# Optimization experiments

Hardware: AMD Instinct MI355X
Metric: run time of the kernel (lower is better)

## Reference

```python
import jax, jax.numpy as jnp
import numpy as np

NUM_HEADS = 16
NEG_INF = -1e24


def setup_inputs() -> dict:
    key = jax.random.key(0)
    k1, k2, k3, k4 = jax.random.split(key, 4)
    T, B, E = 2048, 2, 1024
    std = 0.02
    return {
        "x": jax.random.normal(k1, (T, B, E), dtype=jnp.float32),
        "in_proj_weight": jax.random.normal(k2, (3 * E, E), dtype=jnp.float32) * std,
        "in_proj_bias": jnp.zeros((3 * E,), dtype=jnp.float32),
        "out_w": jax.random.normal(k3, (E, E), dtype=jnp.float32) * std,
        "out_b": jnp.zeros((E,), dtype=jnp.float32),
        "key_padding_mask": jax.random.randint(k4, (T, B), 0, 2) > 0,
    }


def reference(x, in_proj_weight, in_proj_bias, out_w, out_b, key_padding_mask):
    # x: [T, B, E]  (Time x Batch x Channel), self-attention (qkv_same path)
    T, B, E = x.shape
    H = NUM_HEADS
    hd = E // H
    scaling = hd ** -0.5
    qkv = jnp.einsum("tbe,fe->tbf", x, in_proj_weight) + in_proj_bias  # [T,B,3E]
    q, k, v = jnp.split(qkv, 3, axis=-1)
    q = (q * scaling).reshape(T, B, H, hd)
    k = k.reshape(T, B, H, hd)
    v = v.reshape(T, B, H, hd)
    # attention scores: [B, H, T(tgt), S(src)]
    scores = jnp.einsum("tbhd,sbhd->bhts", q, k)
    # key_padding_mask: [S, B] -> broadcast over [B, 1, 1, S]
    pad = key_padding_mask.T[:, None, None, :]
    scores = jnp.where(pad, jnp.float32(NEG_INF), scores)
    attn_weights = jax.nn.softmax(scores, axis=-1)
    # dropout p=0.0 in eval -> identity
    attn = jnp.einsum("bhts,sbhd->tbhd", attn_weights, v).reshape(T, B, E)
    out = jnp.einsum("tbe,fe->tbf", attn, out_w) + out_b
    return out
```

## Files before the change

### kernel.cpp

```cpp
#include <hip/hip_runtime.h>
#include <math.h>

#define T_    2048
#define B_    2
#define E_    1024
#define H_    16
#define HD_   64
#define KD_   1024
#define N3_   3072
#define M_    4096
#define NEGI  -1e24f

typedef __attribute__((ext_vector_type(8))) short          bf16x8;
typedef __attribute__((ext_vector_type(4))) float          f32x4;
typedef __attribute__((ext_vector_type(8))) unsigned short u16x8;

__device__ __forceinline__ unsigned short f2bf(float x) {
    unsigned int u = __float_as_uint(x);
    return (unsigned short)((u + 0x7fffu + ((u >> 16) & 1u)) >> 16);
}

__device__ __forceinline__ void gload16(const unsigned short* g, unsigned short* s) {
    __builtin_amdgcn_global_load_lds(
        (const __attribute__((address_space(1))) void*)g,
        (__attribute__((address_space(3))) void*)s, 16, 0, 0);
}

__global__ __launch_bounds__(256) void cvt_bf16(const float* __restrict__ s,
                                                unsigned short* __restrict__ d, int n4) {
    int i = blockIdx.x * 256 + threadIdx.x;
    if (i >= n4) return;
    float4 v = ((const float4*)s)[i];
    ushort4 o;
    o.x = f2bf(v.x); o.y = f2bf(v.y); o.z = f2bf(v.z); o.w = f2bf(v.w);
    ((ushort4*)d)[i] = o;
}

__global__ __launch_bounds__(256) void build_msk(const int* __restrict__ m,
                                                 float* __restrict__ o) {
    int i = blockIdx.x * 256 + threadIdx.x;
    if (i >= T_ * B_) return;
    o[(i & 1) * T_ + (i >> 1)] = m[i] ? NEGI : 0.f;
}

template <int EPI>
__global__ __launch_bounds__(256) void gemm_mfma(
    const unsigned short* __restrict__ A, const unsigned short* __restrict__ W,
    const float* __restrict__ bias,
    unsigned short* __restrict__ q_o, unsigned short* __restrict__ k_o,
    unsigned short* __restrict__ v_o, float* __restrict__ f_o)
{
    __shared__ __align__(16) unsigned short Ab[128 * 64];
    __shared__ __align__(16) unsigned short Bb[128 * 64];
    const int tid = threadIdx.x;
    const int l = tid & 63, w = tid >> 6;
    const int lr = l & 15, g = l >> 4;
    const int m0 = blockIdx.y * 128, n0 = blockIdx.x * 128;
    const int wr = (w >> 1) * 64, wc = (w & 1) * 64;

    f32x4 acc[4][4];
    #pragma unroll
    for (int i = 0; i < 4; ++i)
        #pragma unroll
        for (int j = 0; j < 4; ++j) acc[i][j] = f32x4{0.f, 0.f, 0.f, 0.f};

    for (int k0 = 0; k0 < KD_; k0 += 64) {
        __syncthreads();
        #pragma unroll
        for (int i = 0; i < 4; ++i) {
            const int fb  = (i * 4 + w) * 64;
            const int row = (fb + l) >> 3;
            const int col = ((l & 7) ^ (row & 7)) * 8;
            gload16(&A[(size_t)(m0 + row) * KD_ + k0 + col], &Ab[fb * 8]);
            gload16(&W[(size_t)(n0 + row) * KD_ + k0 + col], &Bb[fb * 8]);
        }
        __syncthreads();
        #pragma unroll
        for (int ks = 0; ks < 2; ++ks) {
            bf16x8 af[4], bf[4];
            #pragma unroll
            for (int mi = 0; mi < 4; ++mi) {
                const int row = wr + mi * 16 + lr;
                af[mi] = *(const bf16x8*)&Ab[row * 64 + (((ks * 4 + g) ^ (row & 7)) * 8)];
            }
            #pragma unroll
            for (int ni = 0; ni < 4; ++ni) {
                const int row = wc + ni * 16 + lr;
                bf[ni] = *(const bf16x8*)&Bb[row * 64 + (((ks * 4 + g) ^ (row & 7)) * 8)];
            }
            #pragma unroll
            for (int mi = 0; mi < 4; ++mi)
                #pragma unroll
                for (int ni = 0; ni < 4; ++ni)
                    acc[mi][ni] = __builtin_amdgcn_mfma_f32_16x16x32_bf16(
                        af[mi], bf[ni], acc[mi][ni], 0, 0, 0);
        }
    }

    if (EPI == 0) {
        const int sec = n0 >> 10;
        unsigned short* dst = (sec == 0) ? q_o : (sec == 1) ? k_o : v_o;
        const float sc = (sec == 0) ? 0.125f : 1.f;
        #pragma unroll
        for (int ni = 0; ni < 4; ++ni) {
            const int fcol = n0 + wc + ni * 16 + lr;
            const int h = (fcol >> 6) & 15, d = fcol & 63;
            const float bv = bias[fcol];
            #pragma unroll
            for (int mi = 0; mi < 4; ++mi)
                #pragma unroll
                for (int p = 0; p < 4; ++p) {
                    const int m = m0 + wr + mi * 16 + g * 4 + p;
                    const int t = m >> 1, b = m & 1;
                    dst[((size_t)(b * H_ + h) * T_ + t) * HD_ + d] =
                        f2bf((acc[mi][ni][p] + bv) * sc);
                }
        }
    } else {
        #pragma unroll
        for (int ni = 0; ni < 4; ++ni) {
            const int fcol = n0 + wc + ni * 16 + lr;
            const float bv = bias[fcol];
            #pragma unroll
            for (int mi = 0; mi < 4; ++mi)
                #pragma unroll
                for (int p = 0; p < 4; ++p) {
                    const int m = m0 + wr + mi * 16 + g * 4 + p;
                    f_o[(size_t)m * E_ + fcol] = acc[mi][ni][p] + bv;
                }
        }
    }
}

__global__ __launch_bounds__(256) void transpose64(const unsigned short* __restrict__ v,
                                                   unsigned short* __restrict__ vt)
{
    __shared__ __align__(16) unsigned short tile[64][72];
    const int bh = blockIdx.y, t0 = blockIdx.x * 64;
    const int tid = threadIdx.x;
    const int r = tid >> 2, c0 = (tid & 3) * 16;
    const unsigned short* src = v + ((size_t)bh * T_ + t0 + r) * HD_ + c0;
    *(u16x8*)&tile[r][c0]     = *(const u16x8*)&src[0];
    *(u16x8*)&tile[r][c0 + 8] = *(const u16x8*)&src[8];
    __syncthreads();
    u16x8 a, b;
    #pragma unroll
    for (int j = 0; j < 8; ++j) a[j] = tile[c0 + j][r];
    #pragma unroll
    for (int j = 0; j < 8; ++j) b[j] = tile[c0 + 8 + j][r];
    unsigned short* dq = vt + ((size_t)bh * HD_ + r) * T_ + t0 + c0;
    *(u16x8*)&dq[0] = a;
    *(u16x8*)&dq[8] = b;
}

__device__ __forceinline__ void stage64(const unsigned short* src, int ld,
                                        unsigned short* buf, int w, int l) {
    #pragma unroll
    for (int c = 0; c < 2; ++c) {
        const int fb  = (c * 4 + w) * 64;
        const int row = (fb + l) >> 3;
        const int col = ((l & 7) ^ (row & 7)) * 8;
        gload16(src + (size_t)row * ld + col, buf + fb * 8);
    }
}

__global__ __launch_bounds__(256, 3) void attn_mfma(
    const unsigned short* __restrict__ qw, const unsigned short* __restrict__ kw,
    const unsigned short* __restrict__ vtw, const float* __restrict__ msk,
    unsigned short* __restrict__ attn)
{
    __shared__ __align__(16) unsigned short Kb[2][64 * 64];
    __shared__ __align__(16) unsigned short Vb[2][64 * 64];
    __shared__ __align__(16) unsigned short Pb[4][32 * 64];

    const int tid = threadIdx.x;
    const int l = tid & 63, w = tid >> 6;
    const int lr = l & 15, g = l >> 4;
    const int bh = blockIdx.y, b = bh >> 4, h = bh & 15;
    const int q0 = blockIdx.x * 128 + w * 32;

    const unsigned short* kb  = kw  + (size_t)bh * T_ * HD_;
    const unsigned short* vtb = vtw + (size_t)bh * HD_ * T_;
    const float* mb = msk + b * T_;
    unsigned short* Pw = Pb[w];

    bf16x8 qf[2][2];
    #pragma unroll
    for (int qc = 0; qc < 2; ++qc) {
        const unsigned short* qrow = qw + ((size_t)bh * T_ + q0 + qc * 16 + lr) * HD_;
        qf[qc][0] = *(const bf16x8*)&qrow[g * 8];
        qf[qc][1] = *(const bf16x8*)&qrow[32 + g * 8];
    }

    f32x4 o[2][4];
    #pragma unroll
    for (int qc = 0; qc < 2; ++qc)
        #pragma unroll
        for (int df = 0; df < 4; ++df) o[qc][df] = f32x4{0.f, 0.f, 0.f, 0.f};
    float m_run[2] = {-INFINITY, -INFINITY}, l_run[2] = {0.f, 0.f};

    stage64(kb, HD_, Kb[0], w, l);
    stage64(vtb, T_, Vb[0], w, l);
    int cur = 0;

    for (int s0 = 0; s0 < T_; s0 += 64) {
        __syncthreads();
        if (s0 + 64 < T_) {
            stage64(kb + (size_t)(s0 + 64) * HD_, HD_, Kb[cur ^ 1], w, l);
            stage64(vtb + (s0 + 64),          T_, Vb[cur ^ 1], w, l);
        }
        const unsigned short* Kc = Kb[cur];
        const unsigned short* Vc = Vb[cur];

        f32x4 st[4][2];
        #pragma unroll
        for (int sf = 0; sf < 4; ++sf) {
            const int row = sf * 16 + lr;
            const bf16x8 k0v = *(const bf16x8*)&Kc[row * 64 + ((g       ^ (row & 7)) * 8)];
            const bf16x8 k1v = *(const bf16x8*)&Kc[row * 64 + (((4 + g) ^ (row & 7)) * 8)];
            #pragma unroll
            for (int qc = 0; qc < 2; ++qc) {
                f32x4 z = f32x4{0.f, 0.f, 0.f, 0.f};
                z           = __builtin_amdgcn_mfma_f32_16x16x32_bf16(k0v, qf[qc][0], z, 0, 0, 0);
                st[sf][qc]  = __builtin_amdgcn_mfma_f32_16x16x32_bf16(k1v, qf[qc][1], z, 0, 0, 0);
            }
        }
        float4 mv[4];
        #pragma unroll
        for (int sf = 0; sf < 4; ++sf) mv[sf] = *(const float4*)&mb[s0 + sf * 16 + g * 4];

        #pragma unroll
        for (int qc = 0; qc < 2; ++qc) {
            float pmax = -INFINITY;
            #pragma unroll
            for (int sf = 0; sf < 4; ++sf) {
                st[sf][qc][0] += mv[sf].x; st[sf][qc][1] += mv[sf].y;
                st[sf][qc][2] += mv[sf].z; st[sf][qc][3] += mv[sf].w;
                pmax = fmaxf(pmax, fmaxf(fmaxf(st[sf][qc][0], st[sf][qc][1]),
                                         fmaxf(st[sf][qc][2], st[sf][qc][3])));
            }
            pmax = fmaxf(pmax, __shfl_xor(pmax, 16));
            pmax = fmaxf(pmax, __shfl_xor(pmax, 32));
            const float mnew = fmaxf(m_run[qc], pmax);
            const float fac  = __expf(m_run[qc] - mnew);
            float rsum = 0.f;
            unsigned int pk[8];
            #pragma unroll
            for (int sf = 0; sf < 4; ++sf) {
                const float e0 = __expf(st[sf][qc][0] - mnew), e1 = __expf(st[sf][qc][1] - mnew);
                const float e2 = __expf(st[sf][qc][2] - mnew), e3 = __expf(st[sf][qc][3] - mnew);
                rsum += (e0 + e1) + (e2 + e3);
                pk[sf * 2 + 0] = (unsigned int)f2bf(e0) | ((unsigned int)f2bf(e1) << 16);
                pk[sf * 2 + 1] = (unsigned int)f2bf(e2) | ((unsigned int)f2bf(e3) << 16);
            }
            rsum += __shfl_xor(rsum, 16);
            rsum += __shfl_xor(rsum, 32);
            m_run[qc] = mnew;
            l_run[qc] = l_run[qc] * fac + rsum;
            #pragma unroll
            for (int df = 0; df < 4; ++df) {
                o[qc][df][0] *= fac; o[qc][df][1] *= fac;
                o[qc][df][2] *= fac; o[qc][df][3] *= fac;
            }
            const int prow = qc * 16 + lr;
            #pragma unroll
            for (int sf = 0; sf < 4; ++sf) {
                const int blkS = (sf * 2 + (g >> 1)) ^ (prow & 7);
                uint2 val; val.x = pk[sf * 2]; val.y = pk[sf * 2 + 1];
                *(uint2*)&Pw[prow * 64 + blkS * 8 + (g & 1) * 4] = val;
            }
        }

        #pragma unroll
        for (int ks = 0; ks < 2; ++ks) {
            bf16x8 pf[2];
            #pragma unroll
            for (int qc = 0; qc < 2; ++qc) {
                const int prow = qc * 16 + lr;
                pf[qc] = *(const bf16x8*)&Pw[prow * 64 + (((ks * 4 + g) ^ (prow & 7)) * 8)];
            }
            #pragma unroll
            for (int df = 0; df < 4; ++df) {
                const int vrow = df * 16 + lr;
                const bf16x8 vf = *(const bf16x8*)&Vc[vrow * 64 + (((ks * 4 + g) ^ (vrow & 7)) * 8)];
                #pragma unroll
                for (int qc = 0; qc < 2; ++qc)
                    o[qc][df] = __builtin_amdgcn_mfma_f32_16x16x32_bf16(vf, pf[qc], o[qc][df], 0, 0, 0);
            }
        }
        cur ^= 1;
    }

    #pragma unroll
    for (int qc = 0; qc < 2; ++qc) {
        const float inv = 1.f / l_run[qc];
        const int t = q0 + qc * 16 + lr;
        #pragma unroll
        for (int df = 0; df < 4; ++df) {
            ushort4 ov;
            ov.x = f2bf(o[qc][df][0] * inv); ov.y = f2bf(o[qc][df][1] * inv);
            ov.z = f2bf(o[qc][df][2] * inv); ov.w = f2bf(o[qc][df][3] * inv);
            *(ushort4*)&attn[((size_t)t * B_ + b) * E_ + h * HD_ + df * 16 + g * 4] = ov;
        }
    }
}

extern "C" void kernel_launch(void* const* d_in, const int* in_sizes, int n_in,
                              void* d_out, int out_size, void* d_ws, size_t ws_size,
                              hipStream_t stream)
{
    const float* x     = (const float*)d_in[0];
    const float* w_in  = (const float*)d_in[1];
    const float* b_in  = (const float*)d_in[2];
    const float* w_out = (const float*)d_in[3];
    const float* b_out = (const float*)d_in[4];
    const int*   mask  = (const int*)d_in[5];

    const size_t NX = (size_t)M_ * KD_;
    unsigned short* xb   = (unsigned short*)d_ws;
    unsigned short* wib  = xb  + NX;
    unsigned short* wob  = wib + (size_t)N3_ * KD_;
    unsigned short* qb   = wob + (size_t)E_ * KD_;
    unsigned short* kbuf = qb   + NX;
    unsigned short* vbuf = kbuf + NX;
    unsigned short* vtb  = vbuf + NX;
    float*          mskf = (float*)(vtb + NX);
    unsigned short* attnb = xb;

    cvt_bf16<<<(int)(NX / 4 / 256),            256, 0, stream>>>(x,     xb,  (int)(NX / 4));
    cvt_bf16<<<(int)((size_t)N3_*KD_/4/256),   256, 0, stream>>>(w_in,  wib, (int)((size_t)N3_*KD_/4));
    cvt_bf16<<<(int)((size_t)E_*KD_/4/256),    256, 0, stream>>>(w_out, wob, (int)((size_t)E_*KD_/4));
    build_msk<<<(T_*B_ + 255)/256,             256, 0, stream>>>(mask, mskf);

    gemm_mfma<0><<<dim3(N3_/128, M_/128), 256, 0, stream>>>(xb, wib, b_in, qb, kbuf, vbuf, nullptr);
    transpose64 <<<dim3(T_/64, B_*H_),    256, 0, stream>>>(vbuf, vtb);
    attn_mfma   <<<dim3(T_/128, B_*H_),   256, 0, stream>>>(qb, kbuf, vtb, mskf, attnb);
    gemm_mfma<1><<<dim3(E_/128, M_/128),  256, 0, stream>>>(attnb, wob, b_out,
                                                            nullptr, nullptr, nullptr, (float*)d_out);
}
```

Before: 240.2 us.

## Enlarge attention blocks, add lazy softmax rescale, fuse conversions, use packed bf16 cvt

The attention kernel now runs 512-thread blocks covering 256 queries, so each staged K/V tile is shared by eight waves instead of four, with one 16-byte load per thread per tile. The online softmax skips rescaling the accumulators unless the running max would grow by more than 8, saving exp and multiply work per tile. P packing uses the hardware v_cvt_pk_bf16_f32 instruction, and the three fp32-to-bf16 conversion launches are merged into one kernel. Trade-offs are fewer blocks in the attention grid (256 instead of 512), which may reduce occupancy, and a lazy max that lets exponentials reach up to e^8 before any rescale.

```diff
diff --git a/kernel.cpp b/kernel.cpp
--- a/kernel.cpp
+++ b/kernel.cpp
@@ -20,20 +20,34 @@
     return (unsigned short)((u + 0x7fffu + ((u >> 16) & 1u)) >> 16);
 }
 
+__device__ __forceinline__ unsigned int cvtpk_bf16(float a, float b) {
+    unsigned int r;
+    asm("v_cvt_pk_bf16_f32 %0, %1, %2" : "=v"(r) : "v"(a), "v"(b));
+    return r;
+}
+
 __device__ __forceinline__ void gload16(const unsigned short* g, unsigned short* s) {
     __builtin_amdgcn_global_load_lds(
         (const __attribute__((address_space(1))) void*)g,
         (__attribute__((address_space(3))) void*)s, 16, 0, 0);
 }
 
-__global__ __launch_bounds__(256) void cvt_bf16(const float* __restrict__ s,
-                                                unsigned short* __restrict__ d, int n4) {
-    int i = blockIdx.x * 256 + threadIdx.x;
-    if (i >= n4) return;
-    float4 v = ((const float4*)s)[i];
+#define XN4  ((size_t)M_ * KD_ / 4)
+#define WIN4 ((size_t)N3_ * KD_ / 4)
+#define WON4 ((size_t)E_ * KD_ / 4)
+__global__ __launch_bounds__(256) void cvt_all(const float* __restrict__ x,
+                                               const float* __restrict__ wi,
+                                               const float* __restrict__ wo,
+                                               unsigned short* __restrict__ dst) {
+    const size_t i = (size_t)blockIdx.x * 256 + threadIdx.x;
+    const float* s; size_t off;
+    if (i < XN4)             { s = x;  off = i; }
+    else if (i < XN4 + WIN4) { s = wi; off = i - XN4; }
+    else                     { s = wo; off = i - XN4 - WIN4; }
+    float4 v = ((const float4*)s)[off];
     ushort4 o;
     o.x = f2bf(v.x); o.y = f2bf(v.y); o.z = f2bf(v.z); o.w = f2bf(v.w);
-    ((ushort4*)d)[i] = o;
+    ((ushort4*)dst)[i] = o;
 }
 
 __global__ __launch_bounds__(256) void build_msk(const int* __restrict__ m,
@@ -153,31 +167,28 @@
     *(u16x8*)&dq[8] = b;
 }
 
-__device__ __forceinline__ void stage64(const unsigned short* src, int ld,
-                                        unsigned short* buf, int w, int l) {
-    #pragma unroll
-    for (int c = 0; c < 2; ++c) {
-        const int fb  = (c * 4 + w) * 64;
-        const int row = (fb + l) >> 3;
-        const int col = ((l & 7) ^ (row & 7)) * 8;
-        gload16(src + (size_t)row * ld + col, buf + fb * 8);
-    }
-}
-
-__global__ __launch_bounds__(256, 3) void attn_mfma(
+__device__ __forceinline__ void stage8(const unsigned short* src, int ld,
+                                       unsigned short* buf, int w, int l) {
+    const int fb  = w * 64;
+    const int row = (fb + l) >> 3;
+    const int col = ((l & 7) ^ (row & 7)) * 8;
+    gload16(src + (size_t)row * ld + col, buf + fb * 8);
+}
+
+__global__ __launch_bounds__(512, 2) void attn_mfma(
     const unsigned short* __restrict__ qw, const unsigned short* __restrict__ kw,
     const unsigned short* __restrict__ vtw, const float* __restrict__ msk,
     unsigned short* __restrict__ attn)
 {
     __shared__ __align__(16) unsigned short Kb[2][64 * 64];
     __shared__ __align__(16) unsigned short Vb[2][64 * 64];
-    __shared__ __align__(16) unsigned short Pb[4][32 * 64];
+    __shared__ __align__(16) unsigned short Pb[8][32 * 64];
 
     const int tid = threadIdx.x;
     const int l = tid & 63, w = tid >> 6;
     const int lr = l & 15, g = l >> 4;
     const int bh = blockIdx.y, b = bh >> 4, h = bh & 15;
-    const int q0 = blockIdx.x * 128 + w * 32;
+    const int q0 = blockIdx.x * 256 + w * 32;
 
     const unsigned short* kb  = kw  + (size_t)bh * T_ * HD_;
     const unsigned short* vtb = vtw + (size_t)bh * HD_ * T_;
@@ -199,15 +210,15 @@
         for (int df = 0; df < 4; ++df) o[qc][df] = f32x4{0.f, 0.f, 0.f, 0.f};
     float m_run[2] = {-INFINITY, -INFINITY}, l_run[2] = {0.f, 0.f};
 
-    stage64(kb, HD_, Kb[0], w, l);
-    stage64(vtb, T_, Vb[0], w, l);
+    stage8(kb, HD_, Kb[0], w, l);
+    stage8(vtb, T_, Vb[0], w, l);
     int cur = 0;
 
     for (int s0 = 0; s0 < T_; s0 += 64) {
         __syncthreads();
         if (s0 + 64 < T_) {
-            stage64(kb + (size_t)(s0 + 64) * HD_, HD_, Kb[cur ^ 1], w, l);
-            stage64(vtb + (s0 + 64),          T_, Vb[cur ^ 1], w, l);
+            stage8(kb + (size_t)(s0 + 64) * HD_, HD_, Kb[cur ^ 1], w, l);
+            stage8(vtb + (s0 + 64),          T_, Vb[cur ^ 1], w, l);
         }
         const unsigned short* Kc = Kb[cur];
         const unsigned short* Vc = Vb[cur];
@@ -241,27 +252,31 @@
             }
             pmax = fmaxf(pmax, __shfl_xor(pmax, 16));
             pmax = fmaxf(pmax, __shfl_xor(pmax, 32));
-            const float mnew = fmaxf(m_run[qc], pmax);
-            const float fac  = __expf(m_run[qc] - mnew);
+            if (!__all(pmax - m_run[qc] <= 8.f)) {
+                const float mnew = fmaxf(m_run[qc], pmax);
+                const float fac  = __expf(m_run[qc] - mnew);
+                l_run[qc] *= fac;
+                #pragma unroll
+                for (int df = 0; df < 4; ++df) {
+                    o[qc][df][0] *= fac; o[qc][df][1] *= fac;
+                    o[qc][df][2] *= fac; o[qc][df][3] *= fac;
+                }
+                m_run[qc] = mnew;
+            }
+            const float mcur = m_run[qc];
             float rsum = 0.f;
             unsigned int pk[8];
             #pragma unroll
             for (int sf = 0; sf < 4; ++sf) {
-                const float e0 = __expf(st[sf][qc][0] - mnew), e1 = __expf(st[sf][qc][1] - mnew);
-                const float e2 = __expf(st[sf][qc][2] - mnew), e3 = __expf(st[sf][qc][3] - mnew);
+                const float e0 = __expf(st[sf][qc][0] - mcur), e1 = __expf(st[sf][qc][1] - mcur);
+                const float e2 = __expf(st[sf][qc][2] - mcur), e3 = __expf(st[sf][qc][3] - mcur);
                 rsum += (e0 + e1) + (e2 + e3);
-                pk[sf * 2 + 0] = (unsigned int)f2bf(e0) | ((unsigned int)f2bf(e1) << 16);
-                pk[sf * 2 + 1] = (unsigned int)f2bf(e2) | ((unsigned int)f2bf(e3) << 16);
+                pk[sf * 2 + 0] = cvtpk_bf16(e0, e1);
+                pk[sf * 2 + 1] = cvtpk_bf16(e2, e3);
             }
             rsum += __shfl_xor(rsum, 16);
             rsum += __shfl_xor(rsum, 32);
-            m_run[qc] = mnew;
-            l_run[qc] = l_run[qc] * fac + rsum;
-            #pragma unroll
-            for (int df = 0; df < 4; ++df) {
-                o[qc][df][0] *= fac; o[qc][df][1] *= fac;
-                o[qc][df][2] *= fac; o[qc][df][3] *= fac;
-            }
+            l_run[qc] += rsum;
             const int prow = qc * 16 + lr;
             #pragma unroll
             for (int sf = 0; sf < 4; ++sf) {
@@ -327,14 +342,13 @@
     float*          mskf = (float*)(vtb + NX);
     unsigned short* attnb = xb;
 
-    cvt_bf16<<<(int)(NX / 4 / 256),            256, 0, stream>>>(x,     xb,  (int)(NX / 4));
-    cvt_bf16<<<(int)((size_t)N3_*KD_/4/256),   256, 0, stream>>>(w_in,  wib, (int)((size_t)N3_*KD_/4));
-    cvt_bf16<<<(int)((size_t)E_*KD_/4/256),    256, 0, stream>>>(w_out, wob, (int)((size_t)E_*KD_/4));
-    build_msk<<<(T_*B_ + 255)/256,             256, 0, stream>>>(mask, mskf);
+    const int cvt_blocks = (int)((XN4 + WIN4 + WON4) / 256);
+    cvt_all  <<<cvt_blocks,        256, 0, stream>>>(x, w_in, w_out, xb);
+    build_msk<<<(T_*B_ + 255)/256, 256, 0, stream>>>(mask, mskf);
 
     gemm_mfma<0><<<dim3(N3_/128, M_/128), 256, 0, stream>>>(xb, wib, b_in, qb, kbuf, vbuf, nullptr);
     transpose64 <<<dim3(T_/64, B_*H_),    256, 0, stream>>>(vbuf, vtb);
-    attn_mfma   <<<dim3(T_/128, B_*H_),   256, 0, stream>>>(qb, kbuf, vtb, mskf, attnb);
+    attn_mfma   <<<dim3(T_/256, B_*H_),   512, 0, stream>>>(qb, kbuf, vtb, mskf, attnb);
     gemm_mfma<1><<<dim3(E_/128, M_/128),  256, 0, stream>>>(attnb, wob, b_out,
                                                             nullptr, nullptr, nullptr, (float*)d_out);
 }
```

Measured after the change: 230.8 us. -3.9%, faster.
